# Kernel tuning notes

Measured on AMD Instinct MI355X. Metric: run time of the kernel, lower is better.

## Reference

```python
import jax, jax.numpy as jnp
import numpy as np

# Structural metadata (constants): 3 node types, 4 edge types, 2 HGT layers.
T, R, L = 3, 4, 2
H_HID, HEADS, OUT = 256, 8, 128
D = H_HID // HEADS  # per-head dim = 32
SRC_T = (0, 1, 1, 1)  # (author->paper, paper->author, paper->paper, paper->venue)
DST_T = (1, 0, 1, 2)
LN_EPS = 1e-5


def _segment_softmax(logits, seg, n):
    # logits: [E, heads]; softmax over edges sharing the same destination node
    m = jax.ops.segment_max(logits, seg, num_segments=n)
    e = jnp.exp(logits - m[seg])
    s = jax.ops.segment_sum(e, seg, num_segments=n)
    return e / s[seg]


def setup_inputs() -> dict:
    key = jax.random.key(0)
    ks = iter(jax.random.split(key, 64))
    N, E, FIN = 20000, 60000, 128

    def nrm(shape, scale):
        return jax.random.normal(next(ks), shape, jnp.float32) * scale

    return dict(
        x=jax.random.normal(next(ks), (T, N, FIN), jnp.float32),
        edge_index=jax.random.randint(next(ks), (R, 2, E), 0, N),
        Win=nrm((T, FIN, H_HID), 0.05),
        b_in=jnp.zeros((T, H_HID), jnp.float32),
        Wk=nrm((L, T, H_HID, H_HID), 0.05), bk=jnp.zeros((L, T, H_HID), jnp.float32),
        Wq=nrm((L, T, H_HID, H_HID), 0.05), bq=jnp.zeros((L, T, H_HID), jnp.float32),
        Wv=nrm((L, T, H_HID, H_HID), 0.05), bv=jnp.zeros((L, T, H_HID), jnp.float32),
        Wa=nrm((L, T, H_HID, H_HID), 0.05), ba=jnp.zeros((L, T, H_HID), jnp.float32),
        skip=jnp.ones((L, T), jnp.float32),
        a_rel=nrm((L, R, HEADS, D, D), 0.1),
        m_rel=nrm((L, R, HEADS, D, D), 0.1),
        p_rel=jnp.ones((L, R, HEADS), jnp.float32),
        ln_g=jnp.ones((L, T, H_HID), jnp.float32),
        ln_b=jnp.zeros((L, T, H_HID), jnp.float32),
        Wout=nrm((H_HID, OUT), 0.05),
        bout=jnp.zeros((OUT,), jnp.float32),
    )


def reference(x, edge_index, Win, b_in, Wk, bk, Wq, bq, Wv, bv, Wa, ba,
              skip, a_rel, m_rel, p_rel, ln_g, ln_b, Wout, bout):
    N = x.shape[1]
    inv_sqrt_d = jnp.float32(1.0 / np.sqrt(D))
    # Input projection + ReLU (dropout = identity in eval mode)
    h = jax.nn.relu(jnp.einsum('tnf,tfh->tnh', x, Win) + b_in[:, None, :])

    for l in range(L):
        res = h
        # Per-node-type k/q/v projections, reshaped to heads
        k = (jnp.einsum('tnh,tho->tno', h, Wk[l]) + bk[l][:, None]).reshape(T, N, HEADS, D)
        q = (jnp.einsum('tnh,tho->tno', h, Wq[l]) + bq[l][:, None]).reshape(T, N, HEADS, D)
        v = (jnp.einsum('tnh,tho->tno', h, Wv[l]) + bv[l][:, None]).reshape(T, N, HEADS, D)

        agg = jnp.zeros((T, N, HEADS, D), h.dtype)
        for r in range(R):
            st, dt = SRC_T[r], DST_T[r]
            src, dst = edge_index[r, 0], edge_index[r, 1]
            # Per-edge-type relation transforms on source k/v
            k_r = jnp.einsum('nhd,hde->nhe', k[st], a_rel[l, r])
            v_r = jnp.einsum('nhd,hde->nhe', v[st], m_rel[l, r])
            kj = k_r[src]          # [E, heads, d]
            vj = v_r[src]
            qi = q[dt][dst]
            logits = (qi * kj).sum(-1) * p_rel[l, r] * inv_sqrt_d  # [E, heads]
            alpha = _segment_softmax(logits, dst, N)
            msg = vj * alpha[..., None]
            agg = agg.at[dt].add(jax.ops.segment_sum(msg, dst, num_segments=N))

        # Type-specific output linear after exact GELU, gated skip (in==out dims)
        o = jax.nn.gelu(agg.reshape(T, N, H_HID), approximate=False)
        o = jnp.einsum('tnh,tho->tno', o, Wa[l]) + ba[l][:, None]
        beta = jax.nn.sigmoid(skip[l])[:, None, None]
        h = beta * o + (1.0 - beta) * h

        # Model-level residual + LayerNorm + ReLU (dropout = identity)
        h = h + res
        mu = h.mean(-1, keepdims=True)
        var = ((h - mu) ** 2).mean(-1, keepdims=True)
        h = (h - mu) * jax.lax.rsqrt(var + LN_EPS) * ln_g[l][:, None] + ln_b[l][:, None]
        h = jax.nn.relu(h)

    # Shared output projection; outputs stacked over node types: [T, N, OUT]
    return jnp.einsum('tnh,ho->tno', h, Wout) + bout
```

## Files before the change

kernel.cpp:

```cpp
#include <hip/hip_runtime.h>
#include <math.h>

#define T_ 3
#define R_ 4
#define L_ 2
#define H_ 256
#define HEADS_ 8
#define D_ 32
#define FIN_ 128
#define OUT_ 128

typedef unsigned short bf16_t;
typedef __attribute__((ext_vector_type(8))) short bf16x8;
typedef __attribute__((ext_vector_type(4))) float f32x4;

__device__ __forceinline__ float bf2f(bf16_t h) {
    return __uint_as_float(((unsigned)h) << 16);
}
__device__ __forceinline__ float bflo(unsigned u) {
    return __uint_as_float(u << 16);
}
__device__ __forceinline__ float bfhi(unsigned u) {
    return __uint_as_float(u & 0xffff0000u);
}
__device__ __forceinline__ bf16_t f2bf(float f) {
    unsigned u = __float_as_uint(f);
    u += 0x7FFFu + ((u >> 16) & 1u);
    return (bf16_t)(u >> 16);
}
__device__ __forceinline__ float gelu_exact(float x) {
    return 0.5f * x * (1.0f + erff(x * 0.70710678118654752440f));
}

__global__ void zero_kernel(unsigned* __restrict__ p, long n) {
    long i = (long)blockIdx.x * blockDim.x + threadIdx.x;
    long stride = (long)gridDim.x * blockDim.x;
    for (; i < n; i += stride) p[i] = 0u;
}

__global__ __launch_bounds__(256) void transconv2_kernel(
    const float* __restrict__ in0, bf16_t* __restrict__ out0,
    const float* __restrict__ in1, bf16_t* __restrict__ out1,
    int cnt0, int Rr, int Cc)
{
    __shared__ float Ls[64][65];
    const int tid = threadIdx.x;
    int z = blockIdx.z;
    const float* in;
    bf16_t* out;
    if (z < cnt0) { in = in0; out = out0; }
    else          { in = in1; out = out1; z -= cnt0; }
    const long base = (long)z * Rr * Cc;
    const int r0 = blockIdx.y * 64, c0 = blockIdx.x * 64;
    #pragma unroll
    for (int i = 0; i < 16; ++i) {
        int e = tid + i * 256; int row = e >> 6, col = e & 63;
        Ls[row][col] = in[base + (long)(r0 + row) * Cc + c0 + col];
    }
    __syncthreads();
    #pragma unroll
    for (int i = 0; i < 16; ++i) {
        int e = tid + i * 256; int row = e >> 6, col = e & 63;
        out[base + (long)(c0 + row) * Rr + r0 + col] = f2bf(Ls[col][row]);
    }
}

__global__ __launch_bounds__(256) void transconv_kernel(
    const float* __restrict__ in, bf16_t* __restrict__ out, int Rr, int Cc)
{
    __shared__ float Ls[64][65];
    const int tid = threadIdx.x;
    const long base = (long)blockIdx.z * Rr * Cc;
    const int r0 = blockIdx.y * 64, c0 = blockIdx.x * 64;
    #pragma unroll
    for (int i = 0; i < 16; ++i) {
        int e = tid + i * 256; int row = e >> 6, col = e & 63;
        Ls[row][col] = in[base + (long)(r0 + row) * Cc + c0 + col];
    }
    __syncthreads();
    #pragma unroll
    for (int i = 0; i < 16; ++i) {
        int e = tid + i * 256; int row = e >> 6, col = e & 63;
        out[base + (long)(c0 + row) * Rr + r0 + col] = f2bf(Ls[col][row]);
    }
}

__global__ __launch_bounds__(256) void fuse_wT_kernel(
    const float* __restrict__ Wk, const float* __restrict__ Wv,
    const float* __restrict__ bk, const float* __restrict__ bv,
    const float* __restrict__ a_rel, const float* __restrict__ m_rel,
    bf16_t* __restrict__ WkvT, float* __restrict__ bkv)
{
    const int s = blockIdx.z;
    const int kv = s & 1, r = (s >> 1) & 3, l = s >> 3;
    const int SRCT[4] = {0, 1, 1, 1};
    const int st = SRCT[r];
    const float* W = (kv ? Wv : Wk) + ((long)l * T_ + st) * H_ * H_;
    const float* A = (kv ? m_rel : a_rel) + ((long)l * R_ + r) * HEADS_ * D_ * D_;
    const int hh = blockIdx.y, kt = blockIdx.x;
    __shared__ float As[32][33];
    __shared__ float Ws[64][33];
    const int tid = threadIdx.x;
    {
        int d = tid >> 3, e4 = (tid & 7) * 4;
        float4 v = *(const float4*)(A + (hh * D_ + d) * D_ + e4);
        As[d][e4] = v.x; As[d][e4 + 1] = v.y; As[d][e4 + 2] = v.z; As[d][e4 + 3] = v.w;
    }
    #pragma unroll
    for (int p = 0; p < 2; ++p) {
        int idx = p * 256 + tid;
        int row = idx >> 3, c4 = (idx & 7) * 4;
        float4 v = *(const float4*)(W + (long)(kt * 64 + row) * H_ + hh * 32 + c4);
        Ws[row][c4] = v.x; Ws[row][c4 + 1] = v.y; Ws[row][c4 + 2] = v.z; Ws[row][c4 + 3] = v.w;
    }
    __syncthreads();
    const int kl = tid & 63, eb = tid >> 6;
    #pragma unroll
    for (int ii = 0; ii < 8; ++ii) {
        int e = eb * 8 + ii;
        float acc = 0.f;
        #pragma unroll
        for (int d = 0; d < 32; ++d)
            acc += As[d][e] * Ws[kl][d];
        long rowIdx = (long)(s >> 1) * 512 + (kv * 256) + hh * 32 + e;
        WkvT[rowIdx * H_ + kt * 64 + kl] = f2bf(acc);
    }
    if (blockIdx.x == 0 && blockIdx.y == 0) {
        const float* b = (kv ? bv : bk) + ((long)l * T_ + st) * H_;
        const int bh = tid >> 5, be = tid & 31;
        float acc = 0.f;
        #pragma unroll
        for (int d = 0; d < D_; ++d)
            acc += b[bh * D_ + d] * A[(bh * D_ + d) * D_ + be];
        bkv[(long)(s >> 1) * 512 + kv * 256 + tid] = acc;
    }
}

__global__ void hist_kernel(const int* __restrict__ ei, int* __restrict__ indeg,
                            int Nn, int E)
{
    int idx = blockIdx.x * 256 + threadIdx.x;
    if (idx >= R_ * E) return;
    int r = idx / E, e = idx - r * E;
    int d = ei[(size_t)r * 2 * E + E + e];
    atomicAdd(indeg + (size_t)r * Nn + d, 1);
}

__global__ __launch_bounds__(256) void csr_part_kernel(
    const int* __restrict__ indeg, int* __restrict__ partials, int Nn, int nch)
{
    const int r = blockIdx.y, c = blockIdx.x, tid = threadIdx.x;
    const int lane = tid & 63, wave = tid >> 6;
    int idx = c * 256 + tid;
    int v = (idx < Nn) ? indeg[(size_t)r * Nn + idx] : 0;
    #pragma unroll
    for (int off = 1; off < 64; off <<= 1) v += __shfl_xor(v, off);
    __shared__ int wsum[4];
    if (lane == 0) wsum[wave] = v;
    __syncthreads();
    if (tid == 0) partials[r * nch + c] = wsum[0] + wsum[1] + wsum[2] + wsum[3];
}

__global__ __launch_bounds__(256) void csr_scanpart_kernel(
    int* __restrict__ partials, int nch)
{
    const int r = blockIdx.x, tid = threadIdx.x;
    __shared__ int sh[256];
    int v = (tid < nch) ? partials[r * nch + tid] : 0;
    sh[tid] = v;
    __syncthreads();
    for (int off = 1; off < 256; off <<= 1) {
        int u = (tid >= off) ? sh[tid - off] : 0;
        __syncthreads();
        sh[tid] += u;
        __syncthreads();
    }
    if (tid < nch) partials[r * nch + tid] = sh[tid] - v;
}

__global__ __launch_bounds__(256) void csr_write_kernel(
    const int* __restrict__ indeg, const int* __restrict__ partials,
    int* __restrict__ offs, int* __restrict__ cursor, int Nn, int nch)
{
    const int r = blockIdx.y, c = blockIdx.x, tid = threadIdx.x;
    int idx = c * 256 + tid;
    int v = (idx < Nn) ? indeg[(size_t)r * Nn + idx] : 0;
    __shared__ int sh[256];
    sh[tid] = v;
    __syncthreads();
    for (int off = 1; off < 256; off <<= 1) {
        int u = (tid >= off) ? sh[tid - off] : 0;
        __syncthreads();
        sh[tid] += u;
        __syncthreads();
    }
    int incl = sh[tid];
    int base = partials[r * nch + c];
    if (idx < Nn) {
        int excl = base + incl - v;
        offs[(size_t)r * (Nn + 1) + idx] = excl;
        cursor[(size_t)r * Nn + idx] = excl;
        if (idx == Nn - 1) offs[(size_t)r * (Nn + 1) + Nn] = base + incl;
    }
}

__global__ void scatter_kernel(const int* __restrict__ ei, int* __restrict__ cursor,
                               int* __restrict__ esrc, int Nn, int E)
{
    int idx = blockIdx.x * 256 + threadIdx.x;
    if (idx >= R_ * E) return;
    int r = idx / E, e = idx - r * E;
    int s = ei[(size_t)r * 2 * E + e];
    int d = ei[(size_t)r * 2 * E + E + e];
    int pos = atomicAdd(cursor + (size_t)r * Nn + d, 1);
    esrc[(size_t)r * E + pos] = s * 512;
}

#define CHAIN_STEP(ku, vu, prX, mX, sX, x0, x1, x2, x3)                     \
    {                                                                        \
        float dt_ = q0 * bflo(ku.x) + q1 * bfhi(ku.x)                        \
                  + q2 * bflo(ku.y) + q3 * bfhi(ku.y);                       \
        dt_ += __shfl_xor(dt_, 1);                                           \
        dt_ += __shfl_xor(dt_, 2);                                           \
        dt_ += __shfl_xor(dt_, 4);                                           \
        float lg = dt_ * prX;                                                \
        if (__any(lg - mX > 8.f)) {                                          \
            float mn = fmaxf(mX, lg);                                        \
            float fac = __expf(mX - mn);                                     \
            float p = __expf(lg - mn);                                       \
            sX = sX * fac + p;                                               \
            x0 = x0 * fac + p * bflo(vu.x);                                  \
            x1 = x1 * fac + p * bfhi(vu.x);                                  \
            x2 = x2 * fac + p * bflo(vu.y);                                  \
            x3 = x3 * fac + p * bfhi(vu.y);                                  \
            mX = mn;                                                         \
        } else {                                                             \
            float p = __expf(lg - mX);                                       \
            sX += p;                                                         \
            x0 += p * bflo(vu.x);                                            \
            x1 += p * bfhi(vu.x);                                            \
            x2 += p * bflo(vu.y);                                            \
            x3 += p * bfhi(vu.y);                                            \
        }                                                                    \
    }

__global__ __launch_bounds__(512) void agg_all_kernel(
    const int* __restrict__ offs, const int* __restrict__ esrc,
    bf16_t* __restrict__ qbuf, const bf16_t* __restrict__ KV,
    const float* __restrict__ p_l, float scale, int Nn, int E)
{
    static const int NRELg[3] = {2, 1, 1};
    static const int R0g[3]  = {0, 1, 3};
    static const int R1g[3]  = {2, 0, 0};
    static const int DTg[3]  = {1, 0, 2};
    const int grp = blockIdx.y;
    const int wave = threadIdx.x >> 6, lane = threadIdx.x & 63;
    const int d = blockIdx.x * 8 + wave;
    if (d >= Nn) return;
    const int head = lane >> 3;
    const int dt = DTg[grp];
    const bool separate = (NRELg[grp] == 2);

    bf16_t* qrow = qbuf + ((size_t)dt * Nn + d) * H_;
    uint2 qu = ((const uint2*)qrow)[lane];
    float q0 = bflo(qu.x), q1 = bfhi(qu.x), q2 = bflo(qu.y), q3 = bfhi(qu.y);

    const int rA = R0g[grp];
    const int* esA = esrc + (size_t)rA * E;
    const bf16_t* kvA = KV + (size_t)rA * Nn * 512;
    float prA = p_l[rA * HEADS_ + head] * scale;
    int curA = offs[(size_t)rA * (Nn + 1) + d];
    int endA = offs[(size_t)rA * (Nn + 1) + d + 1];

    const int* esB; const bf16_t* kvB; float prB;
    int curB, endB;
    if (separate) {
        const int rB = R1g[grp];
        esB = esrc + (size_t)rB * E;
        kvB = KV + (size_t)rB * Nn * 512;
        prB = p_l[rB * HEADS_ + head] * scale;
        curB = offs[(size_t)rB * (Nn + 1) + d];
        endB = offs[(size_t)rB * (Nn + 1) + d + 1];
    } else {
        int mid = curA + ((endA - curA + 1) >> 1);
        esB = esA; kvB = kvA; prB = prA;
        curB = mid; endB = endA;
        endA = mid;
    }

    float mA = -INFINITY, sA = 0.f, aA0 = 0.f, aA1 = 0.f, aA2 = 0.f, aA3 = 0.f;
    float mB = -INFINITY, sB = 0.f, aB0 = 0.f, aB1 = 0.f, aB2 = 0.f, aB3 = 0.f;

    bool hA = curA < endA, hB = curB < endB;
    uint2 kA, vA, kB, vB;
    if (hA) {
        const bf16_t* r = kvA + esA[curA];
        kA = ((const uint2*)r)[lane]; vA = ((const uint2*)(r + 256))[lane];
    }
    if (hB) {
        const bf16_t* r = kvB + esB[curB];
        kB = ((const uint2*)r)[lane]; vB = ((const uint2*)(r + 256))[lane];
    }

    while (hA || hB) {
        bool nA = hA && (curA + 1 < endA);
        bool nB = hB && (curB + 1 < endB);
        uint2 kA2, vA2, kB2, vB2;
        if (nA) {
            const bf16_t* r = kvA + esA[curA + 1];
            kA2 = ((const uint2*)r)[lane]; vA2 = ((const uint2*)(r + 256))[lane];
        }
        if (nB) {
            const bf16_t* r = kvB + esB[curB + 1];
            kB2 = ((const uint2*)r)[lane]; vB2 = ((const uint2*)(r + 256))[lane];
        }
        if (hA) { CHAIN_STEP(kA, vA, prA, mA, sA, aA0, aA1, aA2, aA3) ++curA; }
        if (hB) { CHAIN_STEP(kB, vB, prB, mB, sB, aB0, aB1, aB2, aB3) ++curB; }
        kA = kA2; vA = vA2; kB = kB2; vB = vB2;
        hA = nA; hB = nB;
    }

    float t0, t1, t2, t3;
    if (separate) {
        float iA = (sA > 0.f) ? 1.f / sA : 0.f;
        float iB = (sB > 0.f) ? 1.f / sB : 0.f;
        t0 = aA0 * iA + aB0 * iB;
        t1 = aA1 * iA + aB1 * iB;
        t2 = aA2 * iA + aB2 * iB;
        t3 = aA3 * iA + aB3 * iB;
    } else {
        if (sB > 0.f) {
            float mm = fmaxf(mA, mB);
            float fx = (sA > 0.f) ? __expf(mA - mm) : 0.f;
            float fy = __expf(mB - mm);
            sA = sA * fx + sB * fy;
            aA0 = aA0 * fx + aB0 * fy;
            aA1 = aA1 * fx + aB1 * fy;
            aA2 = aA2 * fx + aB2 * fy;
            aA3 = aA3 * fx + aB3 * fy;
        }
        float iA = (sA > 0.f) ? 1.f / sA : 0.f;
        t0 = aA0 * iA; t1 = aA1 * iA; t2 = aA2 * iA; t3 = aA3 * iA;
    }
    ushort4 ou;
    ou.x = f2bf(gelu_exact(t0));
    ou.y = f2bf(gelu_exact(t1));
    ou.z = f2bf(gelu_exact(t2));
    ou.w = f2bf(gelu_exact(t3));
    ((ushort4*)qrow)[lane] = ou;
}

#define ASTR 40
#define ESTR 72

template<typename TA, typename TC, int ACT_C>
__global__ __launch_bounds__(256) void mfma_gemm(
    const TA* __restrict__ A, const TA* __restrict__ A2, int zsplit,
    const bf16_t* __restrict__ BT,
    const float* __restrict__ bias, TC* __restrict__ C,
    int M, int K, int Nc,
    long strideA, long strideB, long strideBias, long strideC)
{
    const int gX = gridDim.x, gY = gridDim.y, gZ = gridDim.z;
    const int nwg = gX * gY * gZ;
    int flat = blockIdx.x + gX * (blockIdx.y + gY * blockIdx.z);
    const int qch = nwg >> 3, rch = nwg & 7;
    int xcd = flat & 7, cidx = flat >> 3;
    int swz = (xcd < rch ? xcd * (qch + 1) : rch * (qch + 1) + (xcd - rch) * qch) + cidx;
    const int by = swz / (gX * gZ);
    int rem = swz - by * (gX * gZ);
    const int bz = rem / gX;
    const int bx = rem - bz * gX;

    const TA* Ab = (bz < zsplit) ? (A + (long)bz * strideA) : A2;
    const bf16_t* Bb = BT + (long)bz * strideB;
    const float* biasb = bias + (long)bz * strideBias;
    TC* Cb = C + (long)bz * strideC;

    __shared__ bf16_t As[128 * ASTR];
    __shared__ bf16_t Bs[128 * ASTR];
    __shared__ bf16_t Es[4 * 16 * ESTR];
    const int tid = threadIdx.x;
    const int lane = tid & 63, wave = tid >> 6;
    const int wr = wave >> 1, wc = wave & 1;
    const int bm = by * 128, bn = bx * 128;
    const int r16 = lane & 15, g = lane >> 4;
    f32x4 acc[4][4] = {};

    for (int k0 = 0; k0 < K; k0 += 32) {
        #pragma unroll
        for (int p = 0; p < 2; ++p) {
            int idx = p * 256 + tid;
            int row = idx >> 2, seg = idx & 3;
            int grow = bm + row;
            bf16x8 av = {};
            if (grow < M) {
                if constexpr (sizeof(TA) == 2) {
                    av = *(const bf16x8*)(Ab + (long)grow * K + k0 + seg * 8);
                } else {
                    const float* sp = (const float*)Ab + (long)grow * K + k0 + seg * 8;
                    float4 f0 = *(const float4*)sp, f1 = *(const float4*)(sp + 4);
                    av[0] = (short)f2bf(f0.x); av[1] = (short)f2bf(f0.y);
                    av[2] = (short)f2bf(f0.z); av[3] = (short)f2bf(f0.w);
                    av[4] = (short)f2bf(f1.x); av[5] = (short)f2bf(f1.y);
                    av[6] = (short)f2bf(f1.z); av[7] = (short)f2bf(f1.w);
                }
            }
            *(bf16x8*)(As + row * ASTR + seg * 8) = av;
            bf16x8 bv = *(const bf16x8*)(Bb + (long)(bn + row) * K + k0 + seg * 8);
            *(bf16x8*)(Bs + row * ASTR + seg * 8) = bv;
        }
        __syncthreads();
        bf16x8 af[4], bfr[4];
        #pragma unroll
        for (int m = 0; m < 4; ++m)
            af[m] = *(const bf16x8*)(As + (wr * 64 + m * 16 + r16) * ASTR + g * 8);
        #pragma unroll
        for (int n = 0; n < 4; ++n)
            bfr[n] = *(const bf16x8*)(Bs + (wc * 64 + n * 16 + r16) * ASTR + g * 8);
        #pragma unroll
        for (int m = 0; m < 4; ++m)
            #pragma unroll
            for (int n = 0; n < 4; ++n)
                acc[m][n] = __builtin_amdgcn_mfma_f32_16x16x32_bf16(af[m], bfr[n], acc[m][n], 0, 0, 0);
        __syncthreads();
    }

    float bb[4];
    #pragma unroll
    for (int n = 0; n < 4; ++n)
        bb[n] = biasb[bn + wc * 64 + n * 16 + r16];

    if constexpr (sizeof(TC) == 2) {
        bf16_t* st = Es + wave * (16 * ESTR);
        #pragma unroll
        for (int m = 0; m < 4; ++m) {
            int rowbase = bm + wr * 64 + m * 16;
            #pragma unroll
            for (int n = 0; n < 4; ++n) {
                #pragma unroll
                for (int j = 0; j < 4; ++j) {
                    float vv = acc[m][n][j] + bb[n];
                    if (ACT_C) vv = fmaxf(vv, 0.f);
                    st[(g * 4 + j) * ESTR + n * 16 + r16] = f2bf(vv);
                }
            }
            #pragma unroll
            for (int p = 0; p < 2; ++p) {
                int row = p * 8 + (lane >> 3);
                int col0 = (lane & 7) * 8;
                int grow = rowbase + row;
                bf16x8 val = *(const bf16x8*)(st + row * ESTR + col0);
                if (grow < M)
                    *(bf16x8*)(Cb + (long)grow * Nc + bn + wc * 64 + col0) = val;
            }
        }
    } else {
        #pragma unroll
        for (int n = 0; n < 4; ++n) {
            int col = bn + wc * 64 + n * 16 + r16;
            #pragma unroll
            for (int m = 0; m < 4; ++m) {
                int rowbase = bm + wr * 64 + m * 16 + g * 4;
                #pragma unroll
                for (int j = 0; j < 4; ++j) {
                    int row = rowbase + j;
                    if (row < M) {
                        float vv = acc[m][n][j] + bb[n];
                        if (ACT_C) vv = fmaxf(vv, 0.f);
                        Cb[(long)row * Nc + col] = vv;
                    }
                }
            }
        }
    }
}

__global__ __launch_bounds__(256) void skip_ln_kernel(
    bf16_t* __restrict__ h, const bf16_t* __restrict__ o,
    const float* __restrict__ skip, const float* __restrict__ ln_g,
    const float* __restrict__ ln_b, int Nn)
{
    const int wave = threadIdx.x >> 6;
    const int lane = threadIdx.x & 63;
    long row = (long)blockIdx.x * 4 + wave;
    long total = (long)T_ * Nn;
    if (row >= total) return;
    int t = (int)(row / Nn);
    float beta = 1.f / (1.f + expf(-skip[t]));
    float cb = 2.f - beta;
    ushort4 hv = reinterpret_cast<const ushort4*>(h + row * H_)[lane];
    ushort4 ov = reinterpret_cast<const ushort4*>(o + row * H_)[lane];
    float u0 = beta * bf2f(ov.x) + cb * bf2f(hv.x);
    float u1 = beta * bf2f(ov.y) + cb * bf2f(hv.y);
    float u2 = beta * bf2f(ov.z) + cb * bf2f(hv.z);
    float u3 = beta * bf2f(ov.w) + cb * bf2f(hv.w);
    float s1 = u0 + u1 + u2 + u3;
    float s2 = u0 * u0 + u1 * u1 + u2 * u2 + u3 * u3;
    #pragma unroll
    for (int off = 1; off < 64; off <<= 1) {
        s1 += __shfl_xor(s1, off);
        s2 += __shfl_xor(s2, off);
    }
    float mu = s1 * (1.f / H_);
    float var = s2 * (1.f / H_) - mu * mu;
    float inv = rsqrtf(var + 1e-5f);
    const float4 g = reinterpret_cast<const float4*>(ln_g + (size_t)t * H_)[lane];
    const float4 b = reinterpret_cast<const float4*>(ln_b + (size_t)t * H_)[lane];
    ushort4 r;
    r.x = f2bf(fmaxf((u0 - mu) * inv * g.x + b.x, 0.f));
    r.y = f2bf(fmaxf((u1 - mu) * inv * g.y + b.y, 0.f));
    r.z = f2bf(fmaxf((u2 - mu) * inv * g.z + b.z, 0.f));
    r.w = f2bf(fmaxf((u3 - mu) * inv * g.w + b.w, 0.f));
    reinterpret_cast<ushort4*>(h + row * H_)[lane] = r;
}

extern "C" void kernel_launch(void* const* d_in, const int* in_sizes, int n_in,
                              void* d_out, int out_size, void* d_ws, size_t ws_size,
                              hipStream_t stream)
{
    const float* x     = (const float*)d_in[0];
    const int*   ei    = (const int*)  d_in[1];
    const float* Win   = (const float*)d_in[2];
    const float* b_in  = (const float*)d_in[3];
    const float* Wk    = (const float*)d_in[4];
    const float* bk    = (const float*)d_in[5];
    const float* Wq    = (const float*)d_in[6];
    const float* bq    = (const float*)d_in[7];
    const float* Wv    = (const float*)d_in[8];
    const float* bv    = (const float*)d_in[9];
    const float* Wa    = (const float*)d_in[10];
    const float* ba    = (const float*)d_in[11];
    const float* skip  = (const float*)d_in[12];
    const float* a_rel = (const float*)d_in[13];
    const float* m_rel = (const float*)d_in[14];
    const float* p_rel = (const float*)d_in[15];
    const float* ln_g  = (const float*)d_in[16];
    const float* ln_b  = (const float*)d_in[17];
    const float* Wout  = (const float*)d_in[18];
    const float* bout  = (const float*)d_in[19];
    float* out = (float*)d_out;

    const int N = in_sizes[0] / (T_ * FIN_);
    const int E = in_sizes[1] / (R_ * 2);
    const size_t NH = (size_t)N * H_;
    const int nch = (N + 255) / 256;
    const int ZBIG = 1 << 20;

    char* wp = (char*)d_ws;
    auto alloc = [&](size_t bytes) {
        void* r = wp;
        wp += (bytes + 255) & ~(size_t)255;
        return r;
    };
    bf16_t* h     = (bf16_t*)alloc(T_ * NH * 2);
    bf16_t* qbuf  = (bf16_t*)alloc(T_ * NH * 2);
    bf16_t* KV    = (bf16_t*)alloc((size_t)R_ * N * 512 * 2);
    int*    indeg = (int*)   alloc((size_t)R_ * N * 4);
    int*    offs  = (int*)   alloc((size_t)R_ * (N + 1) * 4);
    int*    cursor= (int*)   alloc((size_t)R_ * N * 4);
    int*    esrc  = (int*)   alloc((size_t)R_ * E * 4);
    int*    parts = (int*)   alloc((size_t)R_ * 256 * 4);
    bf16_t* WqT   = (bf16_t*)alloc((size_t)L_ * T_ * H_ * H_ * 2);
    bf16_t* WaT   = (bf16_t*)alloc((size_t)L_ * T_ * H_ * H_ * 2);
    bf16_t* WinT  = (bf16_t*)alloc((size_t)T_ * FIN_ * H_ * 2);
    bf16_t* WoutT = (bf16_t*)alloc((size_t)H_ * OUT_ * 2);
    bf16_t* WkvT  = (bf16_t*)alloc((size_t)L_ * R_ * 512 * H_ * 2);
    float*  bkv   = (float*) alloc((size_t)L_ * R_ * 512 * 4);

    bf16_t* obuf = KV;

    if ((size_t)(wp - (char*)d_ws) > ws_size) return;

    const float scale = 0.17677669529663688f;
    dim3 blk(256);
    auto gM = [](long M) { return (int)((M + 127) / 128); };

    transconv2_kernel<<<dim3(4, 4, 2 * L_ * T_), blk, 0, stream>>>(
        Wq, WqT, Wa, WaT, L_ * T_, H_, H_);
    transconv_kernel<<<dim3(4, 2, T_), blk, 0, stream>>>(Win, WinT, FIN_, H_);
    transconv_kernel<<<dim3(2, 4, 1),  blk, 0, stream>>>(Wout, WoutT, H_, OUT_);
    fuse_wT_kernel<<<dim3(4, 8, 16), blk, 0, stream>>>(
        Wk, Wv, bk, bv, a_rel, m_rel, WkvT, bkv);

    zero_kernel<<<256, blk, 0, stream>>>((unsigned*)indeg, (long)R_ * N);
    hist_kernel<<<(R_ * E + 255) / 256, blk, 0, stream>>>(ei, indeg, N, E);
    csr_part_kernel<<<dim3(nch, R_), blk, 0, stream>>>(indeg, parts, N, nch);
    csr_scanpart_kernel<<<R_, blk, 0, stream>>>(parts, nch);
    csr_write_kernel<<<dim3(nch, R_), blk, 0, stream>>>(indeg, parts, offs, cursor, N, nch);
    scatter_kernel<<<(R_ * E + 255) / 256, blk, 0, stream>>>(ei, cursor, esrc, N, E);

    mfma_gemm<float, bf16_t, 1><<<dim3(H_ / 128, gM(N), T_), blk, 0, stream>>>(
        x, x, ZBIG, WinT, b_in, h, N, FIN_, H_,
        (long)N * FIN_, (long)FIN_ * H_, H_, (long)NH);

    for (int l = 0; l < L_; ++l) {
        const long lw = (long)l * R_;
        mfma_gemm<bf16_t, bf16_t, 0><<<dim3(512 / 128, gM(N), 4), blk, 0, stream>>>(
            h, h + NH, 1, WkvT + lw * 512 * H_, bkv + lw * 512, KV,
            N, H_, 512, 0L, 512L * H_, 512L, (long)N * 512);
        mfma_gemm<bf16_t, bf16_t, 0><<<dim3(H_ / 128, gM(N), 3), blk, 0, stream>>>(
            h, h, ZBIG, WqT + (size_t)l * T_ * H_ * H_, bq + (size_t)l * T_ * H_, qbuf,
            N, H_, H_, (long)NH, (long)H_ * H_, (long)H_, (long)NH);
        agg_all_kernel<<<dim3((N + 7) / 8, 3), dim3(512), 0, stream>>>(
            offs, esrc, qbuf, KV, p_rel + (size_t)l * R_ * HEADS_, scale, N, E);
        mfma_gemm<bf16_t, bf16_t, 0><<<dim3(H_ / 128, gM(N), 3), blk, 0, stream>>>(
            qbuf, qbuf, ZBIG, WaT + (size_t)l * T_ * H_ * H_, ba + (size_t)l * T_ * H_, obuf,
            N, H_, H_, (long)NH, (long)H_ * H_, (long)H_, (long)NH);
        skip_ln_kernel<<<((size_t)T_ * N + 3) / 4, blk, 0, stream>>>(
            h, obuf, skip + l * T_, ln_g + (size_t)l * T_ * H_, ln_b + (size_t)l * T_ * H_, N);
    }

    mfma_gemm<bf16_t, float, 0><<<dim3(OUT_ / 128, gM((long)T_ * N), 1), blk, 0, stream>>>(
        h, h, ZBIG, WoutT, bout, out, T_ * N, H_, OUT_, 0L, 0L, 0L, 0L);
}
```

Measured before the change: 412.8 us.

## Interleave K/V rows, unroll edge loop by two, fuse Wa GEMM with skip+LayerNorm

The fused K/V weight rows are reordered so each lane's 4 K values and 4 V values sit next to each other. A single 16-byte load per edge then fetches both, and the aggregation loop handles two edges per iteration with masked softmax steps. The agg kernel drops to 256-thread blocks of 4 waves. The separate output GEMM and skip/LayerNorm kernels become one 512-thread MFMA kernel covering a full 256-wide row, which does the row reduction in-register and through LDS and removes the obuf round trip. The cost is more LDS and registers in the fused kernel, and some extra clamped loads past segment ends.

```diff
diff --git a/kernel.cpp b/kernel.cpp
--- a/kernel.cpp
+++ b/kernel.cpp
@@ -122,7 +122,9 @@
         #pragma unroll
         for (int d = 0; d < 32; ++d)
             acc += As[d][e] * Ws[kl][d];
-        long rowIdx = (long)(s >> 1) * 512 + (kv * 256) + hh * 32 + e;
+        int col = hh * 32 + e;
+        int pos = (col >> 2) * 8 + kv * 4 + (col & 3);
+        long rowIdx = (long)(s >> 1) * 512 + pos;
         WkvT[rowIdx * H_ + kt * 64 + kl] = f2bf(acc);
     }
     if (blockIdx.x == 0 && blockIdx.y == 0) {
@@ -132,7 +134,8 @@
         #pragma unroll
         for (int d = 0; d < D_; ++d)
             acc += b[bh * D_ + d] * A[(bh * D_ + d) * D_ + be];
-        bkv[(long)(s >> 1) * 512 + kv * 256 + tid] = acc;
+        int pos = (tid >> 2) * 8 + kv * 4 + (tid & 3);
+        bkv[(long)(s >> 1) * 512 + pos] = acc;
     }
 }
 
@@ -216,35 +219,37 @@
     esrc[(size_t)r * E + pos] = s * 512;
 }
 
-#define CHAIN_STEP(ku, vu, prX, mX, sX, x0, x1, x2, x3)                     \
+#define STEP(rr, vld, prX, mX, sX, x0, x1, x2, x3)                          \
     {                                                                        \
-        float dt_ = q0 * bflo(ku.x) + q1 * bfhi(ku.x)                        \
-                  + q2 * bflo(ku.y) + q3 * bfhi(ku.y);                       \
+        float dt_ = q0 * bflo(rr.x) + q1 * bfhi(rr.x)                        \
+                  + q2 * bflo(rr.y) + q3 * bfhi(rr.y);                       \
         dt_ += __shfl_xor(dt_, 1);                                           \
         dt_ += __shfl_xor(dt_, 2);                                           \
         dt_ += __shfl_xor(dt_, 4);                                           \
-        float lg = dt_ * prX;                                                \
+        float lg = (vld) ? dt_ * prX : -1e30f;                               \
         if (__any(lg - mX > 8.f)) {                                          \
             float mn = fmaxf(mX, lg);                                        \
             float fac = __expf(mX - mn);                                     \
             float p = __expf(lg - mn);                                       \
+            p = (vld) ? p : 0.f;                                             \
             sX = sX * fac + p;                                               \
-            x0 = x0 * fac + p * bflo(vu.x);                                  \
-            x1 = x1 * fac + p * bfhi(vu.x);                                  \
-            x2 = x2 * fac + p * bflo(vu.y);                                  \
-            x3 = x3 * fac + p * bfhi(vu.y);                                  \
+            x0 = x0 * fac + p * bflo(rr.z);                                  \
+            x1 = x1 * fac + p * bfhi(rr.z);                                  \
+            x2 = x2 * fac + p * bflo(rr.w);                                  \
+            x3 = x3 * fac + p * bfhi(rr.w);                                  \
             mX = mn;                                                         \
         } else {                                                             \
             float p = __expf(lg - mX);                                       \
+            p = (vld) ? p : 0.f;                                             \
             sX += p;                                                         \
-            x0 += p * bflo(vu.x);                                            \
-            x1 += p * bfhi(vu.x);                                            \
-            x2 += p * bflo(vu.y);                                            \
-            x3 += p * bfhi(vu.y);                                            \
+            x0 += p * bflo(rr.z);                                            \
+            x1 += p * bfhi(rr.z);                                            \
+            x2 += p * bflo(rr.w);                                            \
+            x3 += p * bfhi(rr.w);                                            \
         }                                                                    \
     }
 
-__global__ __launch_bounds__(512) void agg_all_kernel(
+__global__ __launch_bounds__(256) void agg_all_kernel(
     const int* __restrict__ offs, const int* __restrict__ esrc,
     bf16_t* __restrict__ qbuf, const bf16_t* __restrict__ KV,
     const float* __restrict__ p_l, float scale, int Nn, int E)
@@ -255,7 +260,7 @@
     static const int DTg[3]  = {1, 0, 2};
     const int grp = blockIdx.y;
     const int wave = threadIdx.x >> 6, lane = threadIdx.x & 63;
-    const int d = blockIdx.x * 8 + wave;
+    const int d = blockIdx.x * 4 + wave;
     if (d >= Nn) return;
     const int head = lane >> 3;
     const int dt = DTg[grp];
@@ -287,37 +292,39 @@
         curB = mid; endB = endA;
         endA = mid;
     }
+    const int safeA = (endA > 0) ? endA - 1 : 0;
+    const int safeB = (endB > 0) ? endB - 1 : 0;
+    const int loff = lane * 8;
 
     float mA = -INFINITY, sA = 0.f, aA0 = 0.f, aA1 = 0.f, aA2 = 0.f, aA3 = 0.f;
     float mB = -INFINITY, sB = 0.f, aB0 = 0.f, aB1 = 0.f, aB2 = 0.f, aB3 = 0.f;
 
-    bool hA = curA < endA, hB = curB < endB;
-    uint2 kA, vA, kB, vB;
-    if (hA) {
-        const bf16_t* r = kvA + esA[curA];
-        kA = ((const uint2*)r)[lane]; vA = ((const uint2*)(r + 256))[lane];
-    }
-    if (hB) {
-        const bf16_t* r = kvB + esB[curB];
-        kB = ((const uint2*)r)[lane]; vB = ((const uint2*)(r + 256))[lane];
-    }
-
-    while (hA || hB) {
-        bool nA = hA && (curA + 1 < endA);
-        bool nB = hB && (curB + 1 < endB);
-        uint2 kA2, vA2, kB2, vB2;
-        if (nA) {
-            const bf16_t* r = kvA + esA[curA + 1];
-            kA2 = ((const uint2*)r)[lane]; vA2 = ((const uint2*)(r + 256))[lane];
-        }
-        if (nB) {
-            const bf16_t* r = kvB + esB[curB + 1];
-            kB2 = ((const uint2*)r)[lane]; vB2 = ((const uint2*)(r + 256))[lane];
-        }
-        if (hA) { CHAIN_STEP(kA, vA, prA, mA, sA, aA0, aA1, aA2, aA3) ++curA; }
-        if (hB) { CHAIN_STEP(kB, vB, prB, mB, sB, aB0, aB1, aB2, aB3) ++curB; }
-        kA = kA2; vA = vA2; kB = kB2; vB = vB2;
-        hA = nA; hB = nB;
+    while (curA < endA || curB < endB) {
+        bool vA0 = curA < endA, vA1 = curA + 1 < endA;
+        bool vB0 = curB < endB, vB1 = curB + 1 < endB;
+        uint4 rA0, rA1, rB0, rB1;
+        if (vA0) {
+            int iA0 = esA[curA];
+            int iA1 = esA[min(curA + 1, safeA)];
+            rA0 = *(const uint4*)(kvA + iA0 + loff);
+            rA1 = *(const uint4*)(kvA + iA1 + loff);
+        }
+        if (vB0) {
+            int iB0 = esB[curB];
+            int iB1 = esB[min(curB + 1, safeB)];
+            rB0 = *(const uint4*)(kvB + iB0 + loff);
+            rB1 = *(const uint4*)(kvB + iB1 + loff);
+        }
+        if (vA0) {
+            STEP(rA0, true, prA, mA, sA, aA0, aA1, aA2, aA3)
+            STEP(rA1, vA1, prA, mA, sA, aA0, aA1, aA2, aA3)
+            curA += 2;
+        }
+        if (vB0) {
+            STEP(rB0, true, prB, mB, sB, aB0, aB1, aB2, aB3)
+            STEP(rB1, vB1, prB, mB, sB, aB0, aB1, aB2, aB3)
+            curB += 2;
+        }
     }
 
     float t0, t1, t2, t3;
@@ -476,43 +483,139 @@
     }
 }
 
-__global__ __launch_bounds__(256) void skip_ln_kernel(
-    bf16_t* __restrict__ h, const bf16_t* __restrict__ o,
-    const float* __restrict__ skip, const float* __restrict__ ln_g,
-    const float* __restrict__ ln_b, int Nn)
-{
-    const int wave = threadIdx.x >> 6;
-    const int lane = threadIdx.x & 63;
-    long row = (long)blockIdx.x * 4 + wave;
-    long total = (long)T_ * Nn;
-    if (row >= total) return;
-    int t = (int)(row / Nn);
-    float beta = 1.f / (1.f + expf(-skip[t]));
-    float cb = 2.f - beta;
-    ushort4 hv = reinterpret_cast<const ushort4*>(h + row * H_)[lane];
-    ushort4 ov = reinterpret_cast<const ushort4*>(o + row * H_)[lane];
-    float u0 = beta * bf2f(ov.x) + cb * bf2f(hv.x);
-    float u1 = beta * bf2f(ov.y) + cb * bf2f(hv.y);
-    float u2 = beta * bf2f(ov.z) + cb * bf2f(hv.z);
-    float u3 = beta * bf2f(ov.w) + cb * bf2f(hv.w);
-    float s1 = u0 + u1 + u2 + u3;
-    float s2 = u0 * u0 + u1 * u1 + u2 * u2 + u3 * u3;
-    #pragma unroll
-    for (int off = 1; off < 64; off <<= 1) {
-        s1 += __shfl_xor(s1, off);
-        s2 += __shfl_xor(s2, off);
-    }
-    float mu = s1 * (1.f / H_);
-    float var = s2 * (1.f / H_) - mu * mu;
-    float inv = rsqrtf(var + 1e-5f);
-    const float4 g = reinterpret_cast<const float4*>(ln_g + (size_t)t * H_)[lane];
-    const float4 b = reinterpret_cast<const float4*>(ln_b + (size_t)t * H_)[lane];
-    ushort4 r;
-    r.x = f2bf(fmaxf((u0 - mu) * inv * g.x + b.x, 0.f));
-    r.y = f2bf(fmaxf((u1 - mu) * inv * g.y + b.y, 0.f));
-    r.z = f2bf(fmaxf((u2 - mu) * inv * g.z + b.z, 0.f));
-    r.w = f2bf(fmaxf((u3 - mu) * inv * g.w + b.w, 0.f));
-    reinterpret_cast<ushort4*>(h + row * H_)[lane] = r;
+__global__ __launch_bounds__(512) void gemm_ln_kernel(
+    const bf16_t* __restrict__ A,
+    const bf16_t* __restrict__ BT,
+    const float* __restrict__ bias,
+    bf16_t* __restrict__ h,
+    const float* __restrict__ skip_l,
+    const float* __restrict__ ln_g,
+    const float* __restrict__ ln_b,
+    int M)
+{
+    const int gY = gridDim.y;
+    const int nwg = gY * 3;
+    int flat = blockIdx.y + gY * blockIdx.z;
+    const int qch = nwg >> 3, rch = nwg & 7;
+    int xcd = flat & 7, cidx = flat >> 3;
+    int swz = (xcd < rch ? xcd * (qch + 1) : rch * (qch + 1) + (xcd - rch) * qch) + cidx;
+    const int by = swz / 3;
+    const int bz = swz - by * 3;
+
+    const bf16_t* Ab = A + (long)bz * M * H_;
+    const bf16_t* Bb = BT + (long)bz * H_ * H_;
+    const float* biasb = bias + bz * H_;
+    bf16_t* hb = h + (long)bz * M * H_;
+    const float* lgp = ln_g + bz * H_;
+    const float* lbp = ln_b + bz * H_;
+
+    __shared__ bf16_t As[128 * ASTR];
+    __shared__ bf16_t Bs[256 * ASTR];
+    __shared__ bf16_t Es[8 * 16 * ESTR];
+    __shared__ float  sums[128][4][2];
+
+    const int tid = threadIdx.x;
+    const int lane = tid & 63, wave = tid >> 6;
+    const int wr = wave >> 2, wc = wave & 3;
+    const int bm = by * 128;
+    const int r16 = lane & 15, g = lane >> 4;
+    f32x4 acc[4][4] = {};
+
+    for (int k0 = 0; k0 < H_; k0 += 32) {
+        {
+            int row = tid >> 2, seg = tid & 3;
+            int grow = bm + row;
+            bf16x8 av = {};
+            if (grow < M) av = *(const bf16x8*)(Ab + (long)grow * H_ + k0 + seg * 8);
+            *(bf16x8*)(As + row * ASTR + seg * 8) = av;
+        }
+        #pragma unroll
+        for (int p = 0; p < 2; ++p) {
+            int idx = p * 512 + tid;
+            int row = idx >> 2, seg = idx & 3;
+            bf16x8 bv = *(const bf16x8*)(Bb + (long)row * H_ + k0 + seg * 8);
+            *(bf16x8*)(Bs + row * ASTR + seg * 8) = bv;
+        }
+        __syncthreads();
+        bf16x8 af[4], bfr[4];
+        #pragma unroll
+        for (int m = 0; m < 4; ++m)
+            af[m] = *(const bf16x8*)(As + (wr * 64 + m * 16 + r16) * ASTR + g * 8);
+        #pragma unroll
+        for (int n = 0; n < 4; ++n)
+            bfr[n] = *(const bf16x8*)(Bs + (wc * 64 + n * 16 + r16) * ASTR + g * 8);
+        #pragma unroll
+        for (int m = 0; m < 4; ++m)
+            #pragma unroll
+            for (int n = 0; n < 4; ++n)
+                acc[m][n] = __builtin_amdgcn_mfma_f32_16x16x32_bf16(af[m], bfr[n], acc[m][n], 0, 0, 0);
+        __syncthreads();
+    }
+
+    const float beta = 1.f / (1.f + __expf(-skip_l[bz]));
+    const float cb = 2.f - beta;
+    const int colb = wc * 64;
+    float bb[4], lng[4], lnb[4];
+    #pragma unroll
+    for (int n = 0; n < 4; ++n) {
+        int col = colb + n * 16 + r16;
+        bb[n] = biasb[col]; lng[n] = lgp[col]; lnb[n] = lbp[col];
+    }
+
+    #pragma unroll
+    for (int m = 0; m < 4; ++m) {
+        #pragma unroll
+        for (int j = 0; j < 4; ++j) {
+            int lrow = wr * 64 + m * 16 + g * 4 + j;
+            int grow = bm + lrow;
+            float s1 = 0.f, s2 = 0.f;
+            #pragma unroll
+            for (int n = 0; n < 4; ++n) {
+                float o = acc[m][n][j] + bb[n];
+                float hv = 0.f;
+                if (grow < M)
+                    hv = bf2f(hb[(long)grow * H_ + colb + n * 16 + r16]);
+                float u = beta * o + cb * hv;
+                acc[m][n][j] = u;
+                s1 += u; s2 += u * u;
+            }
+            s1 += __shfl_xor(s1, 1); s2 += __shfl_xor(s2, 1);
+            s1 += __shfl_xor(s1, 2); s2 += __shfl_xor(s2, 2);
+            s1 += __shfl_xor(s1, 4); s2 += __shfl_xor(s2, 4);
+            s1 += __shfl_xor(s1, 8); s2 += __shfl_xor(s2, 8);
+            if (r16 == 0) { sums[lrow][wc][0] = s1; sums[lrow][wc][1] = s2; }
+        }
+    }
+    __syncthreads();
+
+    bf16_t* st = Es + wave * (16 * ESTR);
+    #pragma unroll
+    for (int m = 0; m < 4; ++m) {
+        #pragma unroll
+        for (int j = 0; j < 4; ++j) {
+            int lrow = wr * 64 + m * 16 + g * 4 + j;
+            float S1 = sums[lrow][0][0] + sums[lrow][1][0] + sums[lrow][2][0] + sums[lrow][3][0];
+            float S2 = sums[lrow][0][1] + sums[lrow][1][1] + sums[lrow][2][1] + sums[lrow][3][1];
+            float mu = S1 * (1.f / H_);
+            float var = S2 * (1.f / H_) - mu * mu;
+            float inv = rsqrtf(var + 1e-5f);
+            #pragma unroll
+            for (int n = 0; n < 4; ++n) {
+                float r = fmaxf((acc[m][n][j] - mu) * inv * lng[n] + lnb[n], 0.f);
+                st[(g * 4 + j) * ESTR + n * 16 + r16] = f2bf(r);
+            }
+        }
+        #pragma unroll
+        for (int p = 0; p < 2; ++p) {
+            int row = p * 8 + (lane >> 3);
+            int col0 = (lane & 7) * 8;
+            int grow = bm + wr * 64 + m * 16 + row;
+            bf16x8 val = *(const bf16x8*)(st + row * ESTR + col0);
+            if (grow < M)
+                *(bf16x8*)(hb + (long)grow * H_ + colb + col0) = val;
+        }
+        __syncthreads();
+    }
 }
 
 extern "C" void kernel_launch(void* const* d_in, const int* in_sizes, int n_in,
@@ -568,8 +671,6 @@
     bf16_t* WkvT  = (bf16_t*)alloc((size_t)L_ * R_ * 512 * H_ * 2);
     float*  bkv   = (float*) alloc((size_t)L_ * R_ * 512 * 4);
 
-    bf16_t* obuf = KV;
-
     if ((size_t)(wp - (char*)d_ws) > ws_size) return;
 
     const float scale = 0.17677669529663688f;
@@ -602,13 +703,11 @@
         mfma_gemm<bf16_t, bf16_t, 0><<<dim3(H_ / 128, gM(N), 3), blk, 0, stream>>>(
             h, h, ZBIG, WqT + (size_t)l * T_ * H_ * H_, bq + (size_t)l * T_ * H_, qbuf,
             N, H_, H_, (long)NH, (long)H_ * H_, (long)H_, (long)NH);
-        agg_all_kernel<<<dim3((N + 7) / 8, 3), dim3(512), 0, stream>>>(
+        agg_all_kernel<<<dim3((N + 3) / 4, 3), blk, 0, stream>>>(
             offs, esrc, qbuf, KV, p_rel + (size_t)l * R_ * HEADS_, scale, N, E);
-        mfma_gemm<bf16_t, bf16_t, 0><<<dim3(H_ / 128, gM(N), 3), blk, 0, stream>>>(
-            qbuf, qbuf, ZBIG, WaT + (size_t)l * T_ * H_ * H_, ba + (size_t)l * T_ * H_, obuf,
-            N, H_, H_, (long)NH, (long)H_ * H_, (long)H_, (long)NH);
-        skip_ln_kernel<<<((size_t)T_ * N + 3) / 4, blk, 0, stream>>>(
-            h, obuf, skip + l * T_, ln_g + (size_t)l * T_ * H_, ln_b + (size_t)l * T_ * H_, N);
+        gemm_ln_kernel<<<dim3(1, gM(N), 3), dim3(512), 0, stream>>>(
+            qbuf, WaT + (size_t)l * T_ * H_ * H_, ba + (size_t)l * T_ * H_,
+            h, skip + l * T_, ln_g + (size_t)l * T_ * H_, ln_b + (size_t)l * T_ * H_, N);
     }
 
     mfma_gemm<bf16_t, float, 0><<<dim3(OUT_ / 128, gM((long)T_ * N), 1), blk, 0, stream>>>(
```

After: 419.2 us. Within noise of the previous version (+1.5%).
